# Performance work log

Measured on AMD Instinct MI355X. Metric: run time of the kernel, lower is better.

The kernel has to match this reference:

```python
import jax, jax.numpy as jnp
import numpy as np

B, X, Z, E = 65536, 362, 100, 3  # batch, x_dim, z_dim, action_space


def _lin_init(k, fan_in, fan_out):
    kw, kb = jax.random.split(k)
    bound = 1.0 / np.sqrt(fan_in)
    W = jax.random.uniform(kw, (fan_in, fan_out), jnp.float32, -bound, bound)
    b = jax.random.uniform(kb, (fan_out,), jnp.float32, -bound, bound)
    return W, b


def setup_inputs() -> dict:
    key = jax.random.key(0)
    ks = jax.random.split(key, 12)
    batch_x = jax.random.normal(ks[0], (B, X), jnp.float32)
    batch_next = jax.random.normal(ks[1], (B, X), jnp.float32)
    batch_a = jax.random.randint(ks[2], (B,), 0, E, jnp.int32)
    # encoder params
    W1, b1 = _lin_init(ks[3], X, 256)
    W2, b2 = _lin_init(ks[4], 256, 200)
    W3, b3 = _lin_init(ks[5], 200, Z)
    # stacked expert params [E, in, out]
    def stack(k, fi, fo):
        kk = jax.random.split(k, E)
        Ws, bs = zip(*[_lin_init(kk[i], fi, fo) for i in range(E)])
        return jnp.stack(Ws), jnp.stack(bs)
    eW1, eb1 = stack(ks[6], Z, 150)
    eW2, eb2 = stack(ks[7], 150, 250)
    eW3, eb3 = stack(ks[8], 250, 300)
    eW4, eb4 = stack(ks[9], 300, X)
    return dict(batch_x=batch_x, batch_next=batch_next, batch_a=batch_a,
                W1=W1, b1=b1, W2=W2, b2=b2, W3=W3, b3=b3,
                eW1=eW1, eb1=eb1, eW2=eW2, eb2=eb2,
                eW3=eW3, eb3=eb3, eW4=eW4, eb4=eb4)


def reference(batch_x, batch_next, batch_a,
              W1, b1, W2, b2, W3, b3,
              eW1, eb1, eW2, eb2, eW3, eb3, eW4, eb4):
    # encoder: Linear->ReLU->Linear->ReLU->Linear->Sigmoid
    h = jax.nn.relu(batch_x @ W1 + b1)
    h = jax.nn.relu(h @ W2 + b2)
    z = jax.nn.sigmoid(h @ W3 + b3)  # [B, Z]
    # routed experts: run all E experts on the full batch (E=3, small),
    # then select per-sample output by action index (same math as per-sample loop)
    h = jax.nn.relu(jnp.einsum('bz,ezh->ebh', z, eW1) + eb1[:, None, :])
    h = jax.nn.relu(jnp.einsum('ebh,ehk->ebk', h, eW2) + eb2[:, None, :])
    h = jax.nn.relu(jnp.einsum('ebk,ekm->ebm', h, eW3) + eb3[:, None, :])
    pred_all = jnp.einsum('ebm,emx->ebx', h, eW4) + eb4[:, None, :]  # [E, B, X]
    pred = pred_all[batch_a, jnp.arange(batch_a.shape[0])]  # [B, X]
    delta = batch_next - batch_x
    loss = jnp.mean((pred[:, 1:] - delta[:, 1:]) ** 2) \
         + jnp.mean((pred[:, 0] - delta[:, 0]) ** 2)
    return loss
```

## Files before the change

### kernel.cpp

```cpp
#include <hip/hip_runtime.h>
#include <math.h>

#define BATCH 65536
#define XD 362
#define ZD 100

#define WS_IDX_OFF 256
#define WS_WT_OFF  786688

#define OFF_W1 0
#define OFF_W2 98304
#define OFF_W3 163840
#define OFF_E1 192512
#define OFF_E2 290816
#define OFF_E3 413696
#define OFF_E4 708608

typedef short short8 __attribute__((ext_vector_type(8)));
typedef float f32x4 __attribute__((ext_vector_type(4)));

__device__ __forceinline__ unsigned short f2bf(float f) {
    union { float f; unsigned u; } v; v.f = f;
    unsigned u = v.u + 0x7fffu + ((v.u >> 16) & 1u);
    return (unsigned short)(u >> 16);
}
__device__ __forceinline__ float bf2f(unsigned u) {
    union { unsigned u; float f; } v; v.u = u << 16; return v.f;
}

__global__ __launch_bounds__(256) void repack_kernel(
    const float* __restrict__ W1, const float* __restrict__ W2,
    const float* __restrict__ W3, const float* __restrict__ eW1,
    const float* __restrict__ eW2, const float* __restrict__ eW3,
    const float* __restrict__ eW4, unsigned short* __restrict__ dst) {
    int m = blockIdx.y;
    const float* src; int K, N, Kp, Np; size_t off;
    if (m == 0)      { src = W1; K = 362; N = 256; Kp = 384; Np = 256; off = OFF_W1; }
    else if (m == 1) { src = W2; K = 256; N = 200; Kp = 256; Np = 256; off = OFF_W2; }
    else if (m == 2) { src = W3; K = 200; N = 100; Kp = 224; Np = 128; off = OFF_W3; }
    else if (m <= 5) { int e = m - 3;  src = eW1 + e * 15000;  K = 100; N = 150; Kp = 128; Np = 256; off = OFF_E1 + (size_t)e * 32768; }
    else if (m <= 8) { int e = m - 6;  src = eW2 + e * 37500;  K = 150; N = 250; Kp = 160; Np = 256; off = OFF_E2 + (size_t)e * 40960; }
    else if (m <= 11){ int e = m - 9;  src = eW3 + e * 75000;  K = 250; N = 300; Kp = 256; Np = 384; off = OFF_E3 + (size_t)e * 98304; }
    else             { int e = m - 12; src = eW4 + e * 108600; K = 300; N = 362; Kp = 320; Np = 384; off = OFF_E4 + (size_t)e * 122880; }
    int nkt = Kp / 32;
    int total = Kp * Np;
    for (int i = blockIdx.x * 256 + threadIdx.x; i < total; i += gridDim.x * 256) {
        int j = i & 7, lane = (i >> 3) & 63, t = i >> 9;
        int kt = t % nkt, ct = t / nkt;
        int k = kt * 32 + (lane >> 4) * 8 + j;
        int n = ct * 16 + (lane & 15);
        float v = (k < K && n < N) ? src[(size_t)k * N + n] : 0.0f;
        dst[off + i] = f2bf(v);
    }
}

__global__ __launch_bounds__(256) void bucket_kernel(const int* __restrict__ a,
                                                     int* __restrict__ counts,
                                                     int* __restrict__ idxlist) {
    int b = blockIdx.x * 256 + threadIdx.x;
    int lane = threadIdx.x & 63;
    int e = a[b];
    unsigned long long below = (lane == 63) ? ~0ull >> 1
                                            : ((1ull << (lane + 1)) - 1ull) >> 1;
    int pos = 0;
#pragma unroll
    for (int ee = 0; ee < 3; ++ee) {
        unsigned long long mask = __ballot(e == ee);
        if (e == ee) {
            int leader = __ffsll((long long)mask) - 1;
            int base = 0;
            if (lane == leader)
                base = atomicAdd(&counts[ee], __popcll(mask));
            base = __shfl(base, leader, 64);
            pos = base + __popcll(mask & below);
        }
    }
    idxlist[e * BATCH + pos] = b;
}

template <int KP, int NP, int LDI, int LDO, int NREAL, int NSTORE>
__device__ __forceinline__ void mfma_layer(
    const unsigned short* __restrict__ Wf, const float* __restrict__ bias,
    const unsigned short* __restrict__ inL, unsigned short* __restrict__ outL,
    int wv, int lane) {
    constexpr int NKT = KP / 32, NCT = NP / 16, CPW = NCT / 8;
    const int quad = lane >> 4, l15 = lane & 15;
    f32x4 acc[2][CPW];
#pragma unroll
    for (int rt = 0; rt < 2; ++rt)
#pragma unroll
        for (int i = 0; i < CPW; ++i) acc[rt][i] = (f32x4){0.f, 0.f, 0.f, 0.f};
    const unsigned short* ap = inL + l15 * LDI + quad * 8;
#pragma unroll
    for (int kt = 0; kt < NKT; ++kt) {
        short8 a0 = *(const short8*)(ap + kt * 32);
        short8 a1 = *(const short8*)(ap + 16 * LDI + kt * 32);
        short8 bf[CPW];
#pragma unroll
        for (int i = 0; i < CPW; ++i)
            bf[i] = *(const short8*)(Wf + ((size_t)((wv + 8 * i) * NKT + kt) * 64 + lane) * 8);
#pragma unroll
        for (int i = 0; i < CPW; ++i) {
            acc[0][i] = __builtin_amdgcn_mfma_f32_16x16x32_bf16(a0, bf[i], acc[0][i], 0, 0, 0);
            acc[1][i] = __builtin_amdgcn_mfma_f32_16x16x32_bf16(a1, bf[i], acc[1][i], 0, 0, 0);
        }
    }
#pragma unroll
    for (int i = 0; i < CPW; ++i) {
        int n = (wv + 8 * i) * 16 + l15;
        if (n < NSTORE) {
            float bv = (n < NREAL) ? bias[n] : 0.f;
#pragma unroll
            for (int rt = 0; rt < 2; ++rt)
#pragma unroll
                for (int r = 0; r < 4; ++r) {
                    int row = rt * 16 + quad * 4 + r;
                    float v = fmaxf(acc[rt][i][r] + bv, 0.f);
                    outL[row * LDO + n] = (n < NREAL) ? f2bf(v) : (unsigned short)0;
                }
        }
    }
}

__global__ __launch_bounds__(512, 4) void fused_kernel(
    const float* __restrict__ x, const float* __restrict__ xn,
    const int* __restrict__ counts, const int* __restrict__ idxlist,
    const unsigned short* __restrict__ Wts,
    const float* __restrict__ b1, const float* __restrict__ b2,
    const float* __restrict__ b3, const float* __restrict__ eb1,
    const float* __restrict__ eb2, const float* __restrict__ eb3,
    const float* __restrict__ eb4, float* __restrict__ out) {
    int e = blockIdx.y;
    int cnt = counts[e];
    int start = blockIdx.x * 32;
    if (start >= cnt) return;
    int nrows = min(32, cnt - start);

    __shared__ unsigned short P[32 * 392];
    __shared__ unsigned short Q[32 * 264];
    __shared__ unsigned short R[32 * 328];
    __shared__ int s_idx[32];
    __shared__ float s_part[8];

    int tid = threadIdx.x;
    int wv = tid >> 6, lane = tid & 63;
    const int quad = lane >> 4, l15 = lane & 15;

    if (tid < 32)
        s_idx[tid] = (tid < nrows) ? idxlist[e * BATCH + start + tid] : -1;
    __syncthreads();

    {
        unsigned* dP = (unsigned*)P;
        for (int i = tid; i < 32 * 196; i += 512) {
            int r = i / 196, c = i - r * 196;
            int b = s_idx[r];
            unsigned pk = 0u;
            if (c < 181 && b >= 0) {
                float2 v = *(const float2*)(x + (size_t)b * 362 + 2 * c);
                pk = (unsigned)f2bf(v.x) | ((unsigned)f2bf(v.y) << 16);
            }
            dP[i] = pk;
        }
    }
    __syncthreads();
    mfma_layer<384, 256, 392, 264, 256, 256>(Wts + OFF_W1, b1, P, Q, wv, lane);
    __syncthreads();
    {
        unsigned* dP = (unsigned*)P;
        for (int i = tid; i < 32 * 196; i += 512) {
            int r = i / 196, c = i - r * 196;
            int b = s_idx[r];
            unsigned pk = 0u;
            if (c < 181 && b >= 0) {
                float2 v = *(const float2*)(xn + (size_t)b * 362 + 2 * c);
                unsigned xp = dP[i];
                float x0 = bf2f(xp & 0xffffu), x1 = bf2f(xp >> 16);
                pk = (unsigned)f2bf(v.x - x0) | ((unsigned)f2bf(v.y - x1) << 16);
            }
            dP[i] = pk;
        }
    }
    mfma_layer<256, 256, 264, 264, 200, 224>(Wts + OFF_W2, b2, Q, R, wv, lane);
    __syncthreads();
    {
        const unsigned short* W3f = Wts + OFF_W3;
        f32x4 acc3[2];
#pragma unroll
        for (int rt = 0; rt < 2; ++rt) acc3[rt] = (f32x4){0.f, 0.f, 0.f, 0.f};
        const unsigned short* ap = R + l15 * 264 + quad * 8;
#pragma unroll
        for (int kt = 0; kt < 7; ++kt) {
            short8 a0 = *(const short8*)(ap + kt * 32);
            short8 a1 = *(const short8*)(ap + 16 * 264 + kt * 32);
            short8 bf = *(const short8*)(W3f + ((size_t)(wv * 7 + kt) * 64 + lane) * 8);
            acc3[0] = __builtin_amdgcn_mfma_f32_16x16x32_bf16(a0, bf, acc3[0], 0, 0, 0);
            acc3[1] = __builtin_amdgcn_mfma_f32_16x16x32_bf16(a1, bf, acc3[1], 0, 0, 0);
        }
        int n = wv * 16 + l15;
        float bv = (n < 100) ? b3[n] : 0.f;
#pragma unroll
        for (int rt = 0; rt < 2; ++rt)
#pragma unroll
            for (int r = 0; r < 4; ++r) {
                int row = rt * 16 + quad * 4 + r;
                float s = 1.0f / (1.0f + expf(-(acc3[rt][r] + bv)));
                Q[row * 136 + n] = (n < 100) ? f2bf(s) : (unsigned short)0;
            }
    }
    __syncthreads();
    mfma_layer<128, 256, 136, 168, 150, 160>(Wts + OFF_E1 + (size_t)e * 32768,
                                             eb1 + e * 150, Q, R, wv, lane);
    __syncthreads();
    mfma_layer<160, 256, 168, 264, 250, 256>(Wts + OFF_E2 + (size_t)e * 40960,
                                             eb2 + e * 250, R, Q, wv, lane);
    __syncthreads();
    mfma_layer<256, 384, 264, 328, 300, 320>(Wts + OFF_E3 + (size_t)e * 98304,
                                             eb3 + e * 300, Q, R, wv, lane);
    __syncthreads();

    float lacc = 0.0f;
    {
        constexpr int NKT = 10, CPW = 3;
        const unsigned short* Wf = Wts + OFF_E4 + (size_t)e * 122880;
        const float* bias4 = eb4 + (size_t)e * 362;
        f32x4 acc[2][CPW];
#pragma unroll
        for (int rt = 0; rt < 2; ++rt)
#pragma unroll
            for (int i = 0; i < CPW; ++i) acc[rt][i] = (f32x4){0.f, 0.f, 0.f, 0.f};
        const unsigned short* ap = R + l15 * 328 + quad * 8;
#pragma unroll
        for (int kt = 0; kt < NKT; ++kt) {
            short8 a0 = *(const short8*)(ap + kt * 32);
            short8 a1 = *(const short8*)(ap + 16 * 328 + kt * 32);
            short8 bf[CPW];
#pragma unroll
            for (int i = 0; i < CPW; ++i)
                bf[i] = *(const short8*)(Wf + ((size_t)((wv + 8 * i) * NKT + kt) * 64 + lane) * 8);
#pragma unroll
            for (int i = 0; i < CPW; ++i) {
                acc[0][i] = __builtin_amdgcn_mfma_f32_16x16x32_bf16(a0, bf[i], acc[0][i], 0, 0, 0);
                acc[1][i] = __builtin_amdgcn_mfma_f32_16x16x32_bf16(a1, bf[i], acc[1][i], 0, 0, 0);
            }
        }
        const float WC0 = 1.0f / 65536.0f;
        const float WCR = 1.0f / (361.0f * 65536.0f);
#pragma unroll
        for (int i = 0; i < CPW; ++i) {
            int n = (wv + 8 * i) * 16 + l15;
            if (n < 362) {
                float bv = bias4[n];
                float wgt = (n == 0) ? WC0 : WCR;
#pragma unroll
                for (int rt = 0; rt < 2; ++rt)
#pragma unroll
                    for (int r = 0; r < 4; ++r) {
                        int row = rt * 16 + quad * 4 + r;
                        int b = s_idx[row];
                        if (b >= 0) {
                            float pred = acc[rt][i][r] + bv;
                            float delta = bf2f((unsigned)P[row * 392 + n]);
                            float err = pred - delta;
                            lacc += wgt * err * err;
                        }
                    }
            }
        }
    }
    for (int off = 32; off; off >>= 1)
        lacc += __shfl_down(lacc, off, 64);
    if ((tid & 63) == 0) s_part[wv] = lacc;
    __syncthreads();
    if (tid == 0) {
        float s = 0.f;
#pragma unroll
        for (int i = 0; i < 8; ++i) s += s_part[i];
        atomicAdd(out, s);
    }
}

extern "C" void kernel_launch(void* const* d_in, const int* in_sizes, int n_in,
                              void* d_out, int out_size, void* d_ws, size_t ws_size,
                              hipStream_t stream) {
    const float* x   = (const float*)d_in[0];
    const float* xn  = (const float*)d_in[1];
    const int*   a   = (const int*)d_in[2];
    const float* W1  = (const float*)d_in[3];
    const float* b1  = (const float*)d_in[4];
    const float* W2  = (const float*)d_in[5];
    const float* b2  = (const float*)d_in[6];
    const float* W3  = (const float*)d_in[7];
    const float* b3  = (const float*)d_in[8];
    const float* eW1 = (const float*)d_in[9];
    const float* eb1 = (const float*)d_in[10];
    const float* eW2 = (const float*)d_in[11];
    const float* eb2 = (const float*)d_in[12];
    const float* eW3 = (const float*)d_in[13];
    const float* eb3 = (const float*)d_in[14];
    const float* eW4 = (const float*)d_in[15];
    const float* eb4 = (const float*)d_in[16];

    char* ws = (char*)d_ws;
    int* counts           = (int*)ws;
    int* idxlist          = (int*)(ws + WS_IDX_OFF);
    unsigned short* Wts   = (unsigned short*)(ws + WS_WT_OFF);

    hipMemsetAsync(counts, 0, 256, stream);
    hipMemsetAsync(d_out, 0, sizeof(float), stream);

    repack_kernel<<<dim3(32, 15), 256, 0, stream>>>(W1, W2, W3, eW1, eW2, eW3, eW4, Wts);
    bucket_kernel<<<BATCH / 256, 256, 0, stream>>>(a, counts, idxlist);
    fused_kernel<<<dim3(BATCH / 32, 3), 512, 0, stream>>>(
        x, xn, counts, idxlist, Wts, b1, b2, b3, eb1, eb2, eb3, eb4, (float*)d_out);
}
```

Measured before the change: 423.5 us.

## Drop delta staging buffer to cut LDS and raise occupancy to six blocks

```diff
diff --git a/kernel.cpp b/kernel.cpp
--- a/kernel.cpp
+++ b/kernel.cpp
@@ -122,7 +122,7 @@
     }
 }
 
-__global__ __launch_bounds__(512, 4) void fused_kernel(
+__global__ __launch_bounds__(512, 6) void fused_kernel(
     const float* __restrict__ x, const float* __restrict__ xn,
     const int* __restrict__ counts, const int* __restrict__ idxlist,
     const unsigned short* __restrict__ Wts,
@@ -136,9 +136,8 @@
     if (start >= cnt) return;
     int nrows = min(32, cnt - start);
 
-    __shared__ unsigned short P[32 * 392];
-    __shared__ unsigned short Q[32 * 264];
-    __shared__ unsigned short R[32 * 328];
+    __shared__ unsigned short A[32 * 392];
+    __shared__ unsigned short B[32 * 264];
     __shared__ int s_idx[32];
     __shared__ float s_part[8];
 
@@ -151,7 +150,7 @@
     __syncthreads();
 
     {
-        unsigned* dP = (unsigned*)P;
+        unsigned* dA = (unsigned*)A;
         for (int i = tid; i < 32 * 196; i += 512) {
             int r = i / 196, c = i - r * 196;
             int b = s_idx[r];
@@ -160,35 +159,20 @@
                 float2 v = *(const float2*)(x + (size_t)b * 362 + 2 * c);
                 pk = (unsigned)f2bf(v.x) | ((unsigned)f2bf(v.y) << 16);
             }
-            dP[i] = pk;
-        }
-    }
-    __syncthreads();
-    mfma_layer<384, 256, 392, 264, 256, 256>(Wts + OFF_W1, b1, P, Q, wv, lane);
-    __syncthreads();
-    {
-        unsigned* dP = (unsigned*)P;
-        for (int i = tid; i < 32 * 196; i += 512) {
-            int r = i / 196, c = i - r * 196;
-            int b = s_idx[r];
-            unsigned pk = 0u;
-            if (c < 181 && b >= 0) {
-                float2 v = *(const float2*)(xn + (size_t)b * 362 + 2 * c);
-                unsigned xp = dP[i];
-                float x0 = bf2f(xp & 0xffffu), x1 = bf2f(xp >> 16);
-                pk = (unsigned)f2bf(v.x - x0) | ((unsigned)f2bf(v.y - x1) << 16);
-            }
-            dP[i] = pk;
-        }
-    }
-    mfma_layer<256, 256, 264, 264, 200, 224>(Wts + OFF_W2, b2, Q, R, wv, lane);
+            dA[i] = pk;
+        }
+    }
+    __syncthreads();
+    mfma_layer<384, 256, 392, 264, 256, 256>(Wts + OFF_W1, b1, A, B, wv, lane);
+    __syncthreads();
+    mfma_layer<256, 256, 264, 264, 200, 224>(Wts + OFF_W2, b2, B, A, wv, lane);
     __syncthreads();
     {
         const unsigned short* W3f = Wts + OFF_W3;
         f32x4 acc3[2];
 #pragma unroll
         for (int rt = 0; rt < 2; ++rt) acc3[rt] = (f32x4){0.f, 0.f, 0.f, 0.f};
-        const unsigned short* ap = R + l15 * 264 + quad * 8;
+        const unsigned short* ap = A + l15 * 264 + quad * 8;
 #pragma unroll
         for (int kt = 0; kt < 7; ++kt) {
             short8 a0 = *(const short8*)(ap + kt * 32);
@@ -205,18 +189,18 @@
             for (int r = 0; r < 4; ++r) {
                 int row = rt * 16 + quad * 4 + r;
                 float s = 1.0f / (1.0f + expf(-(acc3[rt][r] + bv)));
-                Q[row * 136 + n] = (n < 100) ? f2bf(s) : (unsigned short)0;
+                B[row * 136 + n] = (n < 100) ? f2bf(s) : (unsigned short)0;
             }
     }
     __syncthreads();
     mfma_layer<128, 256, 136, 168, 150, 160>(Wts + OFF_E1 + (size_t)e * 32768,
-                                             eb1 + e * 150, Q, R, wv, lane);
+                                             eb1 + e * 150, B, A, wv, lane);
     __syncthreads();
     mfma_layer<160, 256, 168, 264, 250, 256>(Wts + OFF_E2 + (size_t)e * 40960,
-                                             eb2 + e * 250, R, Q, wv, lane);
+                                             eb2 + e * 250, A, B, wv, lane);
     __syncthreads();
     mfma_layer<256, 384, 264, 328, 300, 320>(Wts + OFF_E3 + (size_t)e * 98304,
-                                             eb3 + e * 300, Q, R, wv, lane);
+                                             eb3 + e * 300, B, A, wv, lane);
     __syncthreads();
 
     float lacc = 0.0f;
@@ -229,7 +213,7 @@
         for (int rt = 0; rt < 2; ++rt)
 #pragma unroll
             for (int i = 0; i < CPW; ++i) acc[rt][i] = (f32x4){0.f, 0.f, 0.f, 0.f};
-        const unsigned short* ap = R + l15 * 328 + quad * 8;
+        const unsigned short* ap = A + l15 * 328 + quad * 8;
 #pragma unroll
         for (int kt = 0; kt < NKT; ++kt) {
             short8 a0 = *(const short8*)(ap + kt * 32);
@@ -259,9 +243,9 @@
                         int row = rt * 16 + quad * 4 + r;
                         int b = s_idx[row];
                         if (b >= 0) {
-                            float pred = acc[rt][i][r] + bv;
-                            float delta = bf2f((unsigned)P[row * 392 + n]);
-                            float err = pred - delta;
+                            size_t o = (size_t)b * 362 + n;
+                            float delta = xn[o] - x[o];
+                            float err = acc[rt][i][r] + bv - delta;
                             lacc += wgt * err * err;
                         }
                     }
```

Measured after the change: 419.0 us. About the same (-1.1%).
